# Kernel optimization log

Hardware: AMD Instinct MI355X
Metric: run time of the kernel (lower is better)

Reference implementation:

```python
import jax, jax.numpy as jnp
import numpy as np

NUM_OCT, SEMI = 10, 12
FEAT = NUM_OCT * SEMI  # 120
N, K, T = 128, 24, 517
EPS = 1e-5


def setup_inputs() -> dict:
    key = jax.random.key(0)
    ks = jax.random.split(key, 9)
    B, C = 4, 4
    s = 1.0 / np.sqrt(FEAT)
    inp = {
        'x': jax.random.normal(ks[0], (B, C, FEAT, T), dtype=jnp.float32),
        'Wq': jax.random.uniform(ks[1], (N * K, FEAT), jnp.float32, -s, s),
        'bq': jax.random.uniform(ks[2], (N * K,), jnp.float32, -s, s),
        'Wk': jax.random.uniform(ks[3], (N * K, FEAT), jnp.float32, -s, s),
        'bk': jax.random.uniform(ks[4], (N * K,), jnp.float32, -s, s),
        'Wv': jax.random.uniform(ks[5], (N * K, FEAT), jnp.float32, -s, s),
        'bv': jax.random.uniform(ks[6], (N * K,), jnp.float32, -s, s),
        'gamma': jnp.ones((N, T), dtype=jnp.float32),
        'beta': jnp.zeros((N, T), dtype=jnp.float32),
    }
    return inp


def reference(x, Wq, bq, Wk, bk, Wv, bv, gamma, beta):
    B, C, Fd, Tt = x.shape
    BB = B * C
    # [BB, T, FEAT]
    xr = jnp.transpose(x.reshape(BB, Fd, Tt), (0, 2, 1))
    # projections -> [BB, T, K, N] (chunk K heads of width N along channel dim)
    q = (xr @ Wq.T + bq).reshape(BB, Tt, K, N)
    k = (xr @ Wk.T + bk).reshape(BB, Tt, K, N)
    v = (xr @ Wv.T + bv).reshape(BB, Tt, K, N)
    # per-time-step attention over the K heads: [BB, T, K, K]
    wei = jax.nn.softmax(jnp.einsum('btkn,btmn->btkm', q, k), axis=-1)
    out = jnp.einsum('btkm,btmn->btkn', wei, v)  # [BB, T, K, N]
    # permute to [BB, K, N, T] and LayerNorm over last two dims (N, T)
    out = jnp.transpose(out, (0, 2, 3, 1))
    mu = jnp.mean(out, axis=(-2, -1), keepdims=True)
    var = jnp.var(out, axis=(-2, -1), keepdims=True)
    out = (out - mu) * jax.lax.rsqrt(var + EPS) * gamma + beta
    # final permute -> [BB, N, K, T]
    return jnp.transpose(out, (0, 2, 1, 3))
```

## Files before the change

### kernel.cpp

```cpp
#include <hip/hip_runtime.h>
#include <hip/hip_bf16.h>
#include <cstdint>

#define TDIM 517
#define FEATD 120
#define NBB 16
#define NHEAD 24
#define NDIM 128
#define NKC 3072
#define MROWS (NBB * TDIM)
#define MPAD 8320
#define NCOLS (3 * NKC)
#define KPAD 128
#define LN_EPS 1e-5f

typedef short bf16x8 __attribute__((ext_vector_type(8)));
typedef short bf16x4 __attribute__((ext_vector_type(4)));
typedef float f32x4 __attribute__((ext_vector_type(4)));

static __device__ __forceinline__ float bf2f(ushort u) {
  union { uint i; float f; } v; v.i = ((uint)u) << 16; return v.f;
}
static __device__ __forceinline__ ushort f2bf(float f) {
  __hip_bfloat16 h = __float2bfloat16(f);
  return *reinterpret_cast<ushort*>(&h);
}

__global__ __launch_bounds__(256) void convert_x_kernel(
    const float* __restrict__ x, ushort* __restrict__ A)
{
  __shared__ float tile[FEATD][65];
  const int tid = threadIdx.x;
  const int bb = blockIdx.y;
  const int t0 = blockIdx.x * 64;
  const int nt = min(64, TDIM - t0);
  for (int idx = tid; idx < FEATD * 64; idx += 256) {
    int f = idx >> 6, tl = idx & 63;
    if (tl < nt) tile[f][tl] = x[((size_t)bb * FEATD + f) * TDIM + t0 + tl];
  }
  __syncthreads();
  for (int c = tid; c < 64 * 16; c += 256) {
    int tl = c >> 4, c8 = c & 15;
    if (tl >= nt) continue;
    ushort u[8];
    if (c8 < 15) {
#pragma unroll
      for (int j = 0; j < 8; ++j) u[j] = f2bf(tile[c8 * 8 + j][tl]);
    } else {
#pragma unroll
      for (int j = 0; j < 8; ++j) u[j] = 0;
    }
    size_t row = (size_t)bb * TDIM + t0 + tl;
    *reinterpret_cast<uint4*>(A + row * KPAD + c8 * 8) = *reinterpret_cast<const uint4*>(u);
  }
}

__global__ __launch_bounds__(256) void convert_w_kernel(
    const float* __restrict__ Wq, const float* __restrict__ Wk, const float* __restrict__ Wv,
    ushort* __restrict__ B, ushort* __restrict__ A)
{
  const int c = blockIdx.x * 256 + threadIdx.x;
  if (c < NCOLS * 16) {
    int col = c >> 4, c8 = c & 15;
    ushort u[8];
    if (c8 < 15) {
      const float* W = (col < NKC)     ? (Wq + (size_t)col * FEATD)
                     : (col < 2 * NKC) ? (Wk + (size_t)(col - NKC) * FEATD)
                                       : (Wv + (size_t)(col - 2 * NKC) * FEATD);
#pragma unroll
      for (int j = 0; j < 8; ++j) u[j] = f2bf(W[c8 * 8 + j]);
    } else {
#pragma unroll
      for (int j = 0; j < 8; ++j) u[j] = 0;
    }
    *reinterpret_cast<uint4*>(B + (size_t)col * KPAD + c8 * 8) = *reinterpret_cast<const uint4*>(u);
  }
  if (c < (MPAD - MROWS) * 16) {
    uint4 z = {0, 0, 0, 0};
    *reinterpret_cast<uint4*>(A + (size_t)(MROWS + (c >> 4)) * KPAD + (c & 15) * 8) = z;
  }
}

__global__ __launch_bounds__(256) void proj_mfma_kernel(
    const ushort* __restrict__ A, const ushort* __restrict__ B,
    const float* __restrict__ bq, const float* __restrict__ bk, const float* __restrict__ bv,
    ushort* __restrict__ qb, ushort* __restrict__ kb, ushort* __restrict__ vb)
{
  __shared__ __align__(16) ushort sA[128 * KPAD];
  __shared__ __align__(16) ushort sB[128 * KPAD];
  __shared__ float sBias[128];
  const int tid  = threadIdx.x;
  const int lane = tid & 63;
  const int wave = tid >> 6;
  const int wm0  = (wave >> 1) * 64;
  const int wn0  = (wave & 1) * 64;
  const int m0   = blockIdx.x * 128;
  const int n0   = blockIdx.y * 128;
  const int mat  = blockIdx.y / 24;
  const int nloc0 = n0 - mat * NKC;
  const float* bias = (mat == 0) ? bq : (mat == 1) ? bk : bv;
  ushort* outb      = (mat == 0) ? qb : (mat == 1) ? kb : vb;

  if (tid < 128) sBias[tid] = bias[nloc0 + tid];

#pragma unroll
  for (int i = 0; i < 8; ++i) {
    int c = tid + i * 256;
    int row = c >> 4, c8 = c & 15;
    uint4 va = *reinterpret_cast<const uint4*>(A + (size_t)(m0 + row) * KPAD + c8 * 8);
    uint4 vb4 = *reinterpret_cast<const uint4*>(B + (size_t)(n0 + row) * KPAD + c8 * 8);
    *reinterpret_cast<uint4*>(&sA[row * KPAD + ((c8 ^ (row & 7)) << 3)]) = va;
    *reinterpret_cast<uint4*>(&sB[row * KPAD + ((c8 ^ (row & 7)) << 3)]) = vb4;
  }
  __syncthreads();

  f32x4 acc[4][4];
#pragma unroll
  for (int i = 0; i < 4; ++i)
#pragma unroll
    for (int j = 0; j < 4; ++j) acc[i][j] = (f32x4){0.f, 0.f, 0.f, 0.f};

  const int rl = lane & 15;
  const int kg = lane >> 4;
#pragma unroll
  for (int s = 0; s < 4; ++s) {
    bf16x8 af[4], bfr[4];
    const int c8 = s * 4 + kg;
#pragma unroll
    for (int i = 0; i < 4; ++i) {
      int row = wm0 + i * 16 + rl;
      af[i] = *reinterpret_cast<const bf16x8*>(&sA[row * KPAD + ((c8 ^ (row & 7)) << 3)]);
      int rowb = wn0 + i * 16 + rl;
      bfr[i] = *reinterpret_cast<const bf16x8*>(&sB[rowb * KPAD + ((c8 ^ (rowb & 7)) << 3)]);
    }
#pragma unroll
    for (int i = 0; i < 4; ++i)
#pragma unroll
      for (int j = 0; j < 4; ++j)
        acc[i][j] = __builtin_amdgcn_mfma_f32_16x16x32_bf16(af[i], bfr[j], acc[i][j], 0, 0, 0);
  }

  __syncthreads();
  ushort* sC = sA;
#pragma unroll
  for (int i = 0; i < 4; ++i)
#pragma unroll
    for (int j = 0; j < 4; ++j) {
      int col = wn0 + j * 16 + rl;
      float bsv = sBias[col];
#pragma unroll
      for (int r = 0; r < 4; ++r) {
        int row = wm0 + i * 16 + kg * 4 + r;
        sC[row * 128 + col] = f2bf(acc[i][j][r] + bsv);
      }
    }
  __syncthreads();
#pragma unroll
  for (int i = 0; i < 8; ++i) {
    int c = tid + i * 256;
    int row = c >> 4, c8 = c & 15;
    int grow = m0 + row;
    if (grow < MROWS)
      *reinterpret_cast<uint4*>(outb + (size_t)grow * NKC + nloc0 + c8 * 8) =
          *reinterpret_cast<const uint4*>(&sC[row * 128 + c8 * 8]);
  }
}

#define WAVE_LDS 5760
__global__ __launch_bounds__(256) void attn_mfma_kernel(
    const ushort* __restrict__ qb, const ushort* __restrict__ kb,
    const ushort* __restrict__ vb, ushort* __restrict__ obuf,
    float* __restrict__ part)
{
  __shared__ __align__(16) ushort lds[4 * WAVE_LDS];
  const int tid  = threadIdx.x;
  const int wave = tid >> 6;
  const int lane = tid & 63;
  const int c = lane & 15;
  const int g = lane >> 4;
  const int p = blockIdx.x * 4 + wave;
  ushort* vT = lds + wave * WAVE_LDS;
  ushort* wL = vT + 4608;
  const ushort* qp = qb + (size_t)p * NKC;
  const ushort* kp = kb + (size_t)p * NKC;
  const ushort* vp = vb + (size_t)p * NKC;

  uint4 vload[6];
#pragma unroll
  for (int it = 0; it < 6; ++it) {
    int idx = it * 64 + lane;
    int m = idx >> 4, n0 = (idx & 15) * 8;
    vload[it] = *reinterpret_cast<const uint4*>(vp + m * 128 + n0);
  }

  f32x4 sc[2][2];
#pragma unroll
  for (int i = 0; i < 2; ++i)
#pragma unroll
    for (int j = 0; j < 2; ++j) sc[i][j] = (f32x4){0.f, 0.f, 0.f, 0.f};

#pragma unroll
  for (int s = 0; s < 4; ++s) {
    bf16x8 aq[2], bk2[2];
#pragma unroll
    for (int i = 0; i < 2; ++i)
      aq[i] = *reinterpret_cast<const bf16x8*>(qp + (i * 16 + c) * 128 + s * 32 + g * 8);
#pragma unroll
    for (int j = 0; j < 2; ++j)
      bk2[j] = *reinterpret_cast<const bf16x8*>(kp + (j * 16 + c) * 128 + s * 32 + g * 8);
#pragma unroll
    for (int i = 0; i < 2; ++i)
#pragma unroll
      for (int j = 0; j < 2; ++j)
        sc[i][j] = __builtin_amdgcn_mfma_f32_16x16x32_bf16(aq[i], bk2[j], sc[i][j], 0, 0, 0);
  }

#pragma unroll
  for (int i = 0; i < 2; ++i) {
#pragma unroll
    for (int r = 0; r < 4; ++r) {
      float s0 = sc[i][0][r];
      float s1 = (c < 8) ? sc[i][1][r] : -1e30f;
      float mx = fmaxf(s0, s1);
#pragma unroll
      for (int d = 1; d < 16; d <<= 1) mx = fmaxf(mx, __shfl_xor(mx, d));
      float e0 = __expf(s0 - mx);
      float e1 = (c < 8) ? __expf(s1 - mx) : 0.f;
      float sum = e0 + e1;
#pragma unroll
      for (int d = 1; d < 16; d <<= 1) sum += __shfl_xor(sum, d);
      float inv = 1.f / sum;
      int row = i * 16 + g * 4 + r;
      wL[row * 36 + c]      = f2bf(e0 * inv);
      wL[row * 36 + 16 + c] = f2bf(e1 * inv);
    }
  }

#pragma unroll
  for (int it = 0; it < 6; ++it) {
    int idx = it * 64 + lane;
    int m = idx >> 4, n0 = (idx & 15) * 8;
    uint w0 = vload[it].x, w1 = vload[it].y, w2 = vload[it].z, w3 = vload[it].w;
    vT[(n0 + 0) * 36 + m] = (ushort)(w0 & 0xffff);
    vT[(n0 + 1) * 36 + m] = (ushort)(w0 >> 16);
    vT[(n0 + 2) * 36 + m] = (ushort)(w1 & 0xffff);
    vT[(n0 + 3) * 36 + m] = (ushort)(w1 >> 16);
    vT[(n0 + 4) * 36 + m] = (ushort)(w2 & 0xffff);
    vT[(n0 + 5) * 36 + m] = (ushort)(w2 >> 16);
    vT[(n0 + 6) * 36 + m] = (ushort)(w3 & 0xffff);
    vT[(n0 + 7) * 36 + m] = (ushort)(w3 >> 16);
  }
#pragma unroll
  for (int h = 0; h < 16; ++h) {
    int idx = h * 64 + lane;
    int n = idx >> 3, mm = 24 + (idx & 7);
    vT[n * 36 + mm] = 0;
  }

  union FU { bf16x4 h[2]; bf16x8 v; };
  bf16x8 wa[2];
#pragma unroll
  for (int i = 0; i < 2; ++i) {
    FU u;
    u.h[0] = *reinterpret_cast<const bf16x4*>(wL + (i * 16 + c) * 36 + g * 8);
    u.h[1] = *reinterpret_cast<const bf16x4*>(wL + (i * 16 + c) * 36 + g * 8 + 4);
    wa[i] = u.v;
  }

  float ls0[4] = {0.f, 0.f, 0.f, 0.f}, ls20[4] = {0.f, 0.f, 0.f, 0.f};
  float ls1[4] = {0.f, 0.f, 0.f, 0.f}, ls21[4] = {0.f, 0.f, 0.f, 0.f};
  ushort* op = obuf + (size_t)p * NKC;
#pragma unroll
  for (int nb = 0; nb < 8; ++nb) {
    FU u;
    const ushort* vrow = vT + (nb * 16 + c) * 36 + g * 8;
    u.h[0] = *reinterpret_cast<const bf16x4*>(vrow);
    u.h[1] = *reinterpret_cast<const bf16x4*>(vrow + 4);
    bf16x8 vf = u.v;
#pragma unroll
    for (int i = 0; i < 2; ++i) {
      f32x4 pv = (f32x4){0.f, 0.f, 0.f, 0.f};
      pv = __builtin_amdgcn_mfma_f32_16x16x32_bf16(wa[i], vf, pv, 0, 0, 0);
      if (i == 0) {
#pragma unroll
        for (int q = 0; q < 4; ++q) {
          op[(g * 4 + q) * 128 + nb * 16 + c] = f2bf(pv[q]);
          ls0[q] += pv[q];
          ls20[q] += pv[q] * pv[q];
        }
      } else if (g < 2) {
#pragma unroll
        for (int q = 0; q < 4; ++q) {
          op[(16 + g * 4 + q) * 128 + nb * 16 + c] = f2bf(pv[q]);
          ls1[q] += pv[q];
          ls21[q] += pv[q] * pv[q];
        }
      }
    }
  }

#pragma unroll
  for (int q = 0; q < 4; ++q) {
#pragma unroll
    for (int d = 1; d < 16; d <<= 1) {
      ls0[q]  += __shfl_xor(ls0[q], d);
      ls20[q] += __shfl_xor(ls20[q], d);
      ls1[q]  += __shfl_xor(ls1[q], d);
      ls21[q] += __shfl_xor(ls21[q], d);
    }
  }
  if (c == 0) {
    float* pr = part + (size_t)p * 48;
#pragma unroll
    for (int q = 0; q < 4; ++q) {
      int kk = g * 4 + q;
      pr[2 * kk]     = ls0[q];
      pr[2 * kk + 1] = ls20[q];
    }
    if (g < 2) {
#pragma unroll
      for (int q = 0; q < 4; ++q) {
        int kk = 16 + g * 4 + q;
        pr[2 * kk]     = ls1[q];
        pr[2 * kk + 1] = ls21[q];
      }
    }
  }
}

__global__ __launch_bounds__(256) void ln_part_reduce_kernel(
    const float* __restrict__ part, float* __restrict__ stats)
{
  const int b = blockIdx.x;
  const int bb = b / NHEAD, kk = b % NHEAD;
  const int tid = threadIdx.x;
  float s = 0.f, s2 = 0.f;
  for (int tt = tid; tt < TDIM; tt += 256) {
    const float* pr = part + ((size_t)(bb * TDIM + tt)) * 48 + 2 * kk;
    s += pr[0];
    s2 += pr[1];
  }
  __shared__ float rs[256], rs2[256];
  rs[tid] = s; rs2[tid] = s2;
  __syncthreads();
  for (int off = 128; off > 0; off >>= 1) {
    if (tid < off) { rs[tid] += rs[tid + off]; rs2[tid] += rs2[tid + off]; }
    __syncthreads();
  }
  if (tid == 0) {
    const float inv = 1.f / (NDIM * TDIM);
    float mu = rs[0] * inv;
    float var = rs2[0] * inv - mu * mu;
    stats[b] = mu;
    stats[384 + b] = rsqrtf(var + LN_EPS);
  }
}

__global__ __launch_bounds__(256) void transpose_apply_kernel(
    const ushort* __restrict__ obuf, const float* __restrict__ stats,
    const float* __restrict__ gamma, const float* __restrict__ beta,
    float* __restrict__ out)
{
  __shared__ float tileF[256 * 32];
  const int tid = threadIdx.x;
  const int bb = blockIdx.z, kk = blockIdx.y;
  const int nq = blockIdx.x / 3, ch = blockIdx.x % 3;
  const int nb = nq * 32;
  const int t0 = ch * 256;
  const float mu = stats[bb * NHEAD + kk];
  const float rstd = stats[384 + bb * NHEAD + kk];

  if (ch < 2) {
#pragma unroll
    for (int i = 0; i < 4; ++i) {
      int idx = tid + i * 256;
      int tl = idx >> 2, n8 = (idx & 3) * 8;
      uint4 v = *reinterpret_cast<const uint4*>(
          obuf + ((size_t)(bb * TDIM + t0 + tl)) * NKC + kk * NDIM + nb + n8);
      const ushort* u = reinterpret_cast<const ushort*>(&v);
#pragma unroll
      for (int j = 0; j < 8; ++j) {
        int nl = n8 + j;
        int col = (nl + (tl & 31) + (tl >> 5)) & 31;
        tileF[tl * 32 + col] = bf2f(u[j]);
      }
    }
    __syncthreads();

#pragma unroll
    for (int p = 0; p < 4; ++p) {
      int nl = p * 8 + (tid >> 5);
      int n = nb + nl;
      int tpos = tid & 31;
#pragma unroll
      for (int s = 0; s < 2; ++s) {
        int tg = t0 + s * 128 + tpos * 4;
        const size_t gb = (size_t)n * TDIM + tg;
        float g4[4], b4[4], vals[4];
        __builtin_memcpy(g4, &gamma[gb], 16);
        __builtin_memcpy(b4, &beta[gb], 16);
#pragma unroll
        for (int j = 0; j < 4; ++j) {
          int tl = s * 128 + tpos * 4 + j;
          int col = (nl + (tl & 31) + (tl >> 5)) & 31;
          vals[j] = (tileF[tl * 32 + col] - mu) * rstd * g4[j] + b4[j];
        }
        __builtin_memcpy(out + (((size_t)bb * NDIM + n) * NHEAD + kk) * TDIM + tg,
                         vals, 16);
      }
    }
  } else {
    for (int c2 = tid; c2 < 32 * 5; c2 += 256) {
      int nl = c2 / 5, tl = c2 % 5;
      int n = nb + nl, tg = 512 + tl;
      float v = bf2f(obuf[((size_t)(bb * TDIM + tg)) * NKC + kk * NDIM + n]);
      out[(((size_t)bb * NDIM + n) * NHEAD + kk) * TDIM + tg] =
          (v - mu) * rstd * gamma[(size_t)n * TDIM + tg] +
          beta[(size_t)n * TDIM + tg];
    }
  }
}

extern "C" void kernel_launch(void* const* d_in, const int* in_sizes, int n_in,
                              void* d_out, int out_size, void* d_ws, size_t ws_size,
                              hipStream_t stream) {
  const float* x     = (const float*)d_in[0];
  const float* Wq    = (const float*)d_in[1];
  const float* bq    = (const float*)d_in[2];
  const float* Wk    = (const float*)d_in[3];
  const float* bk    = (const float*)d_in[4];
  const float* Wv    = (const float*)d_in[5];
  const float* bv    = (const float*)d_in[6];
  const float* gamma = (const float*)d_in[7];
  const float* beta  = (const float*)d_in[8];
  float* out = (float*)d_out;

  char* wsb = (char*)d_ws;
  float* stats = (float*)wsb;
  ushort* A = (ushort*)(wsb + 4096);
  ushort* B = A + (size_t)MPAD * KPAD;
  ushort* qb = B + (size_t)NCOLS * KPAD;
  ushort* kb = qb + (size_t)MROWS * NKC;
  ushort* vb = kb + (size_t)MROWS * NKC;
  ushort* obuf = vb + (size_t)MROWS * NKC;
  float* part = (float*)(obuf + (size_t)MROWS * NKC);

  convert_x_kernel<<<dim3(9, NBB), 256, 0, stream>>>(x, A);
  convert_w_kernel<<<(NCOLS * 16 + 255) / 256, 256, 0, stream>>>(Wq, Wk, Wv, B, A);
  proj_mfma_kernel<<<dim3(MPAD / 128, NCOLS / 128), 256, 0, stream>>>(
      A, B, bq, bk, bv, qb, kb, vb);
  attn_mfma_kernel<<<MROWS / 4, 256, 0, stream>>>(qb, kb, vb, obuf, part);
  ln_part_reduce_kernel<<<NBB * NHEAD, 256, 0, stream>>>(part, stats);
  transpose_apply_kernel<<<dim3(12, NHEAD, NBB), 256, 0, stream>>>(
      obuf, stats, gamma, beta, out);
}
```

Baseline: 158.1 us.

## Merge conversion kernels and fold LN stat reduction into apply kernel

Combines the x and weight bf16 conversion kernels into one launch with a block-index split. Removes the separate LayerNorm partial-reduce kernel: each transpose/apply block now recomputes the per-(bb,head) mean and rstd from the attention partials itself. Also vectorizes the zero-fill of the padded vT columns in the attention kernel. This cuts two launches and a global round-trip for the stats, at the cost of redundant reductions (12 blocks per head) and extra syncs in the apply kernel.

```diff
diff --git a/kernel.cpp b/kernel.cpp
--- a/kernel.cpp
+++ b/kernel.cpp
@@ -26,58 +26,59 @@
   return *reinterpret_cast<ushort*>(&h);
 }
 
-__global__ __launch_bounds__(256) void convert_x_kernel(
-    const float* __restrict__ x, ushort* __restrict__ A)
+__global__ __launch_bounds__(256) void convert_kernel(
+    const float* __restrict__ x,
+    const float* __restrict__ Wq, const float* __restrict__ Wk, const float* __restrict__ Wv,
+    ushort* __restrict__ A, ushort* __restrict__ B)
 {
   __shared__ float tile[FEATD][65];
   const int tid = threadIdx.x;
-  const int bb = blockIdx.y;
-  const int t0 = blockIdx.x * 64;
-  const int nt = min(64, TDIM - t0);
-  for (int idx = tid; idx < FEATD * 64; idx += 256) {
-    int f = idx >> 6, tl = idx & 63;
-    if (tl < nt) tile[f][tl] = x[((size_t)bb * FEATD + f) * TDIM + t0 + tl];
-  }
-  __syncthreads();
-  for (int c = tid; c < 64 * 16; c += 256) {
-    int tl = c >> 4, c8 = c & 15;
-    if (tl >= nt) continue;
-    ushort u[8];
-    if (c8 < 15) {
-#pragma unroll
-      for (int j = 0; j < 8; ++j) u[j] = f2bf(tile[c8 * 8 + j][tl]);
-    } else {
-#pragma unroll
-      for (int j = 0; j < 8; ++j) u[j] = 0;
-    }
-    size_t row = (size_t)bb * TDIM + t0 + tl;
-    *reinterpret_cast<uint4*>(A + row * KPAD + c8 * 8) = *reinterpret_cast<const uint4*>(u);
-  }
-}
-
-__global__ __launch_bounds__(256) void convert_w_kernel(
-    const float* __restrict__ Wq, const float* __restrict__ Wk, const float* __restrict__ Wv,
-    ushort* __restrict__ B, ushort* __restrict__ A)
-{
-  const int c = blockIdx.x * 256 + threadIdx.x;
-  if (c < NCOLS * 16) {
-    int col = c >> 4, c8 = c & 15;
-    ushort u[8];
-    if (c8 < 15) {
-      const float* W = (col < NKC)     ? (Wq + (size_t)col * FEATD)
-                     : (col < 2 * NKC) ? (Wk + (size_t)(col - NKC) * FEATD)
-                                       : (Wv + (size_t)(col - 2 * NKC) * FEATD);
-#pragma unroll
-      for (int j = 0; j < 8; ++j) u[j] = f2bf(W[c8 * 8 + j]);
-    } else {
-#pragma unroll
-      for (int j = 0; j < 8; ++j) u[j] = 0;
-    }
-    *reinterpret_cast<uint4*>(B + (size_t)col * KPAD + c8 * 8) = *reinterpret_cast<const uint4*>(u);
-  }
-  if (c < (MPAD - MROWS) * 16) {
-    uint4 z = {0, 0, 0, 0};
-    *reinterpret_cast<uint4*>(A + (size_t)(MROWS + (c >> 4)) * KPAD + (c & 15) * 8) = z;
+  const int b = blockIdx.x;
+
+  if (b < 144) {
+    const int bb = b / 9;
+    const int t0 = (b % 9) * 64;
+    const int nt = min(64, TDIM - t0);
+    for (int idx = tid; idx < FEATD * 64; idx += 256) {
+      int f = idx >> 6, tl = idx & 63;
+      if (tl < nt) tile[f][tl] = x[((size_t)bb * FEATD + f) * TDIM + t0 + tl];
+    }
+    __syncthreads();
+    for (int c = tid; c < 64 * 16; c += 256) {
+      int tl = c >> 4, c8 = c & 15;
+      if (tl >= nt) continue;
+      ushort u[8];
+      if (c8 < 15) {
+#pragma unroll
+        for (int j = 0; j < 8; ++j) u[j] = f2bf(tile[c8 * 8 + j][tl]);
+      } else {
+#pragma unroll
+        for (int j = 0; j < 8; ++j) u[j] = 0;
+      }
+      size_t row = (size_t)bb * TDIM + t0 + tl;
+      *reinterpret_cast<uint4*>(A + row * KPAD + c8 * 8) = *reinterpret_cast<const uint4*>(u);
+    }
+  } else {
+    const int c = (b - 144) * 256 + tid;
+    if (c < NCOLS * 16) {
+      int col = c >> 4, c8 = c & 15;
+      ushort u[8];
+      if (c8 < 15) {
+        const float* W = (col < NKC)     ? (Wq + (size_t)col * FEATD)
+                       : (col < 2 * NKC) ? (Wk + (size_t)(col - NKC) * FEATD)
+                                         : (Wv + (size_t)(col - 2 * NKC) * FEATD);
+#pragma unroll
+        for (int j = 0; j < 8; ++j) u[j] = f2bf(W[c8 * 8 + j]);
+      } else {
+#pragma unroll
+        for (int j = 0; j < 8; ++j) u[j] = 0;
+      }
+      *reinterpret_cast<uint4*>(B + (size_t)col * KPAD + c8 * 8) = *reinterpret_cast<const uint4*>(u);
+    }
+    if (c < (MPAD - MROWS) * 16) {
+      uint4 z = {0, 0, 0, 0};
+      *reinterpret_cast<uint4*>(A + (size_t)(MROWS + (c >> 4)) * KPAD + (c & 15) * 8) = z;
+    }
   }
 }
 
@@ -251,10 +252,11 @@
     vT[(n0 + 7) * 36 + m] = (ushort)(w3 >> 16);
   }
 #pragma unroll
-  for (int h = 0; h < 16; ++h) {
+  for (int h = 0; h < 4; ++h) {
     int idx = h * 64 + lane;
-    int n = idx >> 3, mm = 24 + (idx & 7);
-    vT[n * 36 + mm] = 0;
+    int n = idx >> 1, half = idx & 1;
+    uint2 z2 = {0, 0};
+    *reinterpret_cast<uint2*>(vT + n * 36 + 24 + half * 4) = z2;
   }
 
   union FU { bf16x4 h[2]; bf16x8 v; };
@@ -328,47 +330,18 @@
   }
 }
 
-__global__ __launch_bounds__(256) void ln_part_reduce_kernel(
-    const float* __restrict__ part, float* __restrict__ stats)
-{
-  const int b = blockIdx.x;
-  const int bb = b / NHEAD, kk = b % NHEAD;
-  const int tid = threadIdx.x;
-  float s = 0.f, s2 = 0.f;
-  for (int tt = tid; tt < TDIM; tt += 256) {
-    const float* pr = part + ((size_t)(bb * TDIM + tt)) * 48 + 2 * kk;
-    s += pr[0];
-    s2 += pr[1];
-  }
-  __shared__ float rs[256], rs2[256];
-  rs[tid] = s; rs2[tid] = s2;
-  __syncthreads();
-  for (int off = 128; off > 0; off >>= 1) {
-    if (tid < off) { rs[tid] += rs[tid + off]; rs2[tid] += rs2[tid + off]; }
-    __syncthreads();
-  }
-  if (tid == 0) {
-    const float inv = 1.f / (NDIM * TDIM);
-    float mu = rs[0] * inv;
-    float var = rs2[0] * inv - mu * mu;
-    stats[b] = mu;
-    stats[384 + b] = rsqrtf(var + LN_EPS);
-  }
-}
-
 __global__ __launch_bounds__(256) void transpose_apply_kernel(
-    const ushort* __restrict__ obuf, const float* __restrict__ stats,
+    const ushort* __restrict__ obuf, const float* __restrict__ part,
     const float* __restrict__ gamma, const float* __restrict__ beta,
     float* __restrict__ out)
 {
   __shared__ float tileF[256 * 32];
+  __shared__ float rs[256], rs2[256];
   const int tid = threadIdx.x;
   const int bb = blockIdx.z, kk = blockIdx.y;
   const int nq = blockIdx.x / 3, ch = blockIdx.x % 3;
   const int nb = nq * 32;
   const int t0 = ch * 256;
-  const float mu = stats[bb * NHEAD + kk];
-  const float rstd = stats[384 + bb * NHEAD + kk];
 
   if (ch < 2) {
 #pragma unroll
@@ -385,8 +358,27 @@
         tileF[tl * 32 + col] = bf2f(u[j]);
       }
     }
+  }
+
+  {
+    float s = 0.f, s2 = 0.f;
+    for (int tt = tid; tt < TDIM; tt += 256) {
+      const float* pr = part + ((size_t)(bb * TDIM + tt)) * 48 + 2 * kk;
+      s += pr[0];
+      s2 += pr[1];
+    }
+    rs[tid] = s; rs2[tid] = s2;
+  }
+  __syncthreads();
+  for (int off = 128; off > 0; off >>= 1) {
+    if (tid < off) { rs[tid] += rs[tid + off]; rs2[tid] += rs2[tid + off]; }
     __syncthreads();
-
+  }
+  const float invN = 1.f / (NDIM * TDIM);
+  const float mu = rs[0] * invN;
+  const float rstd = rsqrtf(rs2[0] * invN - mu * mu + LN_EPS);
+
+  if (ch < 2) {
 #pragma unroll
     for (int p = 0; p < 4; ++p) {
       int nl = p * 8 + (tid >> 5);
@@ -436,7 +428,6 @@
   float* out = (float*)d_out;
 
   char* wsb = (char*)d_ws;
-  float* stats = (float*)wsb;
   ushort* A = (ushort*)(wsb + 4096);
   ushort* B = A + (size_t)MPAD * KPAD;
   ushort* qb = B + (size_t)NCOLS * KPAD;
@@ -445,12 +436,10 @@
   ushort* obuf = vb + (size_t)MROWS * NKC;
   float* part = (float*)(obuf + (size_t)MROWS * NKC);
 
-  convert_x_kernel<<<dim3(9, NBB), 256, 0, stream>>>(x, A);
-  convert_w_kernel<<<(NCOLS * 16 + 255) / 256, 256, 0, stream>>>(Wq, Wk, Wv, B, A);
+  convert_kernel<<<720, 256, 0, stream>>>(x, Wq, Wk, Wv, A, B);
   proj_mfma_kernel<<<dim3(MPAD / 128, NCOLS / 128), 256, 0, stream>>>(
       A, B, bq, bk, bv, qb, kb, vb);
   attn_mfma_kernel<<<MROWS / 4, 256, 0, stream>>>(qb, kb, vb, obuf, part);
-  ln_part_reduce_kernel<<<NBB * NHEAD, 256, 0, stream>>>(part, stats);
   transpose_apply_kernel<<<dim3(12, NHEAD, NBB), 256, 0, stream>>>(
-      obuf, stats, gamma, beta, out);
-}
+      obuf, part, gamma, beta, out);
+}
```

New measurement: 156.1 us. Within noise of the previous version (-1.3%).
